# Kernel optimization log

Hardware: AMD Instinct MI355X
Metric: run time of the kernel (lower is better)

## Reference

```python
import jax, jax.numpy as jnp
import numpy as np

DIM = 768

def setup_inputs() -> dict:
    key = jax.random.key(0)
    k1, k2, k3, k4 = jax.random.split(key, 4)
    B, N, C = 32, 577, DIM
    x = jax.random.normal(k1, (B, N, C), dtype=jnp.float32)
    # torch Linear weights: (out_features, in_features)
    w_qkv = jax.random.normal(k2, (3 * C, C), dtype=jnp.float32) * (C ** -0.5)
    w_proj = jax.random.normal(k3, (C, C), dtype=jnp.float32) * (C ** -0.5)
    b_proj = jax.random.normal(k4, (C,), dtype=jnp.float32) * 0.02
    return {"x": x, "w_qkv": w_qkv, "w_proj": w_proj, "b_proj": b_proj}

def reference(x, w_qkv, w_proj, b_proj):
    B, N, C = x.shape
    attn_size = int((N - 1) ** 0.5)
    scale = C ** -0.5
    qkv = (x @ w_qkv.T).reshape(B, N, 3, C)          # [B,N,3,C]
    qkv = jnp.transpose(qkv, (2, 0, 1, 3))           # [3,B,N,C]
    q, k, v = qkv[0], qkv[1], qkv[2]
    attn = jax.nn.softmax(jnp.einsum('bnc,bmc->bnm', q, k) * scale, axis=-1)  # [B,N,N]
    y = jnp.einsum('bnm,bmc->bnc', attn, v)          # [B,N,C]
    # faithful to original: transpose(1,2) then reshape back (data permutation)
    y = jnp.transpose(y, (0, 2, 1)).reshape(B, N, C)
    out = y @ w_proj.T + b_proj
    token_attn = attn[:, 0, 1:].reshape(B, 1, attn_size, attn_size)
    return (out, token_attn)
```

## Files before the change

kernel.cpp:

```cpp
#include <hip/hip_runtime.h>


typedef __attribute__((ext_vector_type(4))) float f32x4;
typedef __attribute__((ext_vector_type(8))) short short8;
typedef __attribute__((ext_vector_type(8))) unsigned short ushort8v;
typedef __attribute__((ext_vector_type(4))) unsigned short ushort4v;

#define TILE 128
#define BK 64

#define NB 32
#define SEQ 577
#define SEQP 640
#define DIM 768
#define MTOT (NB * SEQ)
#define VTLD (NB * SEQP)
#define KC 0.05205949529797614f

__device__ __forceinline__ unsigned short f2bf(float f) {
  union { float f; unsigned u; } x; x.f = f;
  unsigned r = x.u + 0x7fffu + ((x.u >> 16) & 1u);
  return (unsigned short)(r >> 16);
}

__device__ __forceinline__ float bf2f(unsigned short v) {
  union { unsigned u; float f; } x; x.u = ((unsigned)v) << 16; return x.f;
}

__device__ __forceinline__ void gload16(const unsigned short* g, unsigned short* l) {
  __builtin_amdgcn_global_load_lds(
      (const __attribute__((address_space(1))) unsigned int*)g,
      (__attribute__((address_space(3))) unsigned int*)l, 16, 0, 0);
}

__device__ __forceinline__ int swiz(int lin, int nblk) {
  int xcd = lin & 7, pos = lin >> 3;
  int per = nblk >> 3, rem = nblk & 7;
  return xcd * per + (xcd < rem ? xcd : rem) + pos;
}

__device__ __forceinline__ void gemm_core(
    unsigned short* smem,
    const unsigned short* __restrict__ A, int ldA, int rowmaxA, int blkM,
    const unsigned short* __restrict__ B, int ldB, int rowmaxB, int blkN,
    int K, f32x4 acc[4][4])
{
  unsigned short* sA = smem;
  unsigned short* sB = smem + TILE * BK;
  const int t = threadIdx.x;
  const int lane = t & 63;
  const int wave = t >> 6;
  const int wr = (wave >> 1) * 64;
  const int wc = (wave & 1) * 64;
  const int lrow = lane & 15;
  const int quad = lane >> 4;

  for (int k0 = 0; k0 < K; k0 += BK) {
#pragma unroll
    for (int it = 0; it < 4; ++it) {
      int tt = t + it * 256;
      int rr = tt >> 3;
      int gc = (tt & 7) ^ (rr & 7);
      int ra = blkM + rr; if (ra > rowmaxA) ra = rowmaxA;
      int rb = blkN + rr; if (rb > rowmaxB) rb = rowmaxB;
      gload16(A + (size_t)ra * ldA + k0 + gc * 8, sA + tt * 8);
      gload16(B + (size_t)rb * ldB + k0 + gc * 8, sB + tt * 8);
    }
    __syncthreads();
#pragma unroll
    for (int kk = 0; kk < 2; ++kk) {
      short8 af[4], bfr[4];
#pragma unroll
      for (int i = 0; i < 4; ++i) {
        int m = wr + i * 16 + lrow;
        af[i] = *(const short8*)(sA + m * BK + (((kk * 4 + quad) ^ (m & 7)) * 8));
      }
#pragma unroll
      for (int j = 0; j < 4; ++j) {
        int n = wc + j * 16 + lrow;
        bfr[j] = *(const short8*)(sB + n * BK + (((kk * 4 + quad) ^ (n & 7)) * 8));
      }
#pragma unroll
      for (int i = 0; i < 4; ++i)
#pragma unroll
        for (int j = 0; j < 4; ++j)
          acc[i][j] = __builtin_amdgcn_mfma_f32_16x16x32_bf16(af[i], bfr[j], acc[i][j], 0, 0, 0);
    }
    __syncthreads();
  }
}

#define N4X  3545088
#define N4W1 442368
#define N4W2 147456
__global__ __launch_bounds__(256) void k_cvt3(
    const float* __restrict__ x, const float* __restrict__ w1, const float* __restrict__ w2,
    unsigned short* __restrict__ xo, unsigned short* __restrict__ w1o,
    unsigned short* __restrict__ w2o) {
  int i = blockIdx.x * 256 + threadIdx.x;
  const float4* src; ushort4* dst; int off;
  if (i < N4X)                 { src = (const float4*)x;  dst = (ushort4*)xo;  off = i; }
  else if (i < N4X + N4W1)     { src = (const float4*)w1; dst = (ushort4*)w1o; off = i - N4X; }
  else                         { src = (const float4*)w2; dst = (ushort4*)w2o; off = i - N4X - N4W1; }
  float4 v = src[off];
  ushort4 o;
  o.x = f2bf(v.x); o.y = f2bf(v.y); o.z = f2bf(v.z); o.w = f2bf(v.w);
  dst[off] = o;
}

__global__ __launch_bounds__(256, 2) void k_qkv(
    const unsigned short* __restrict__ xb, const unsigned short* __restrict__ wb,
    unsigned short* __restrict__ qb, unsigned short* __restrict__ kb,
    unsigned short* __restrict__ vt) {
  __shared__ unsigned short smem[2 * TILE * BK];
  f32x4 acc[4][4];
#pragma unroll
  for (int i = 0; i < 4; ++i)
#pragma unroll
    for (int j = 0; j < 4; ++j) acc[i][j] = (f32x4){0.f, 0.f, 0.f, 0.f};

  int lin = swiz(blockIdx.y * 18 + blockIdx.x, 18 * 160);
  const int tN = lin % 18;
  const int tMall = lin / 18;
  const int b = tMall / 5;
  const int mt = tMall % 5;
  const int sel = tN / 6, cbase = (tN % 6) * TILE;
  const unsigned short* Xb = xb + (size_t)b * SEQ * DIM;

  const int t = threadIdx.x, lane = t & 63, wave = t >> 6;
  const int wr = (wave >> 1) * 64, wc = (wave & 1) * 64;
  const int l15 = lane & 15, quad = lane >> 4;

  if (sel < 2) {
    gemm_core(smem, Xb, DIM, SEQ - 1, mt * TILE, wb, DIM, 3 * DIM - 1, tN * TILE, DIM, acc);
#pragma unroll
    for (int i = 0; i < 4; ++i)
#pragma unroll
      for (int j = 0; j < 4; ++j)
#pragma unroll
        for (int r = 0; r < 4; ++r) {
          int m = wr + i * 16 + quad * 4 + r, n = wc + j * 16 + l15;
          smem[m * TILE + (n ^ ((m & 7) << 3))] = f2bf(acc[i][j][r]);
        }
    __syncthreads();
    unsigned short* dst = sel == 0 ? qb : kb;
#pragma unroll
    for (int s = 0; s < 8; ++s) {
      int idx = t + s * 256, rr = idx >> 4, seg = idx & 15;
      int nn = mt * TILE + rr;
      if (nn < SEQ) {
        ushort8v v = *(const ushort8v*)(smem + rr * TILE + ((seg * 8) ^ ((rr & 7) << 3)));
        *(ushort8v*)(dst + ((size_t)(b * SEQ + nn)) * DIM + cbase + seg * 8) = v;
      }
    }
  } else {
    gemm_core(smem, wb, DIM, 3 * DIM - 1, 2 * DIM + cbase, Xb, DIM, SEQ - 1, mt * TILE, DIM, acc);
#pragma unroll
    for (int i = 0; i < 4; ++i)
#pragma unroll
      for (int j = 0; j < 4; ++j)
#pragma unroll
        for (int r = 0; r < 4; ++r) {
          int m = wr + i * 16 + quad * 4 + r, n = wc + j * 16 + l15;
          smem[m * TILE + (n ^ ((m & 7) << 3))] = f2bf(acc[i][j][r]);
        }
    __syncthreads();
#pragma unroll
    for (int s = 0; s < 8; ++s) {
      int idx = t + s * 256, rr = idx >> 4, seg = idx & 15;
      int c = cbase + rr;
      int n0 = mt * TILE + seg * 8;
      if (n0 < SEQ) {
        ushort8v v = *(const ushort8v*)(smem + rr * TILE + ((seg * 8) ^ ((rr & 7) << 3)));
        unsigned short* dp = vt + (size_t)c * VTLD + (size_t)b * SEQP + n0;
        if (n0 + 8 <= SEQ) *(ushort8v*)dp = v;
        else {
#pragma unroll
          for (int e = 0; e < 8; ++e) if (n0 + e < SEQ) dp[e] = v[e];
        }
      }
    }
  }
}

__global__ __launch_bounds__(256, 2) void k_logits(
    const unsigned short* __restrict__ qb, const unsigned short* __restrict__ kb,
    unsigned short* __restrict__ Pt, float* __restrict__ part) {
  __shared__ unsigned short smem[2 * TILE * BK];
  __shared__ float rpart[128][2];
  f32x4 acc[4][4];
#pragma unroll
  for (int i = 0; i < 4; ++i)
#pragma unroll
    for (int j = 0; j < 4; ++j) acc[i][j] = (f32x4){0.f, 0.f, 0.f, 0.f};
  int lin = swiz(blockIdx.y * 25 + blockIdx.x, 25 * NB);
  const int b = lin / 25;
  const int tM = (lin % 25) / 5, tN = lin % 5;
  const unsigned short* A = qb + (size_t)b * SEQ * DIM;
  const unsigned short* B = kb + (size_t)b * SEQ * DIM;
  gemm_core(smem, A, DIM, SEQ - 1, tM * TILE, B, DIM, SEQ - 1, tN * TILE, DIM, acc);

  const int t = threadIdx.x, lane = t & 63, wave = t >> 6;
  const int wr = (wave >> 1) * 64, wc = (wave & 1) * 64;
  const int l15 = lane & 15, quad = lane >> 4;

#pragma unroll
  for (int i = 0; i < 4; ++i)
#pragma unroll
    for (int j = 0; j < 4; ++j) {
      int ng = tN * TILE + wc + j * 16 + l15;
#pragma unroll
      for (int r = 0; r < 4; ++r) {
        float e = exp2f(acc[i][j][r] * KC);
        acc[i][j][r] = (ng < SEQ) ? e : 0.f;
      }
    }
#pragma unroll
  for (int i = 0; i < 4; ++i)
#pragma unroll
    for (int r = 0; r < 4; ++r) {
      float p = acc[i][0][r] + acc[i][1][r] + acc[i][2][r] + acc[i][3][r];
      p += __shfl_xor(p, 1); p += __shfl_xor(p, 2);
      p += __shfl_xor(p, 4); p += __shfl_xor(p, 8);
      if (l15 == 0) rpart[wr + i * 16 + quad * 4 + r][wave & 1] = p;
    }
  __syncthreads();
  if (t < 128) {
    int row = tM * TILE + t;
    part[((size_t)b * 5 + tN) * SEQP + row] = rpart[t][0] + rpart[t][1];
  }
#pragma unroll
  for (int i = 0; i < 4; ++i)
#pragma unroll
    for (int j = 0; j < 4; ++j)
#pragma unroll
      for (int r = 0; r < 4; ++r) {
        int m = wr + i * 16 + quad * 4 + r, n = wc + j * 16 + l15;
        smem[m * TILE + (n ^ ((m & 7) << 3))] = f2bf(acc[i][j][r]);
      }
  __syncthreads();
  unsigned short* Pb = Pt + (size_t)b * SEQP * SEQP;
#pragma unroll
  for (int s = 0; s < 8; ++s) {
    int idx = t + s * 256, rr = idx >> 4, seg = idx & 15;
    int m = tM * TILE + rr;
    ushort8v v = *(const ushort8v*)(smem + rr * TILE + ((seg * 8) ^ ((rr & 7) << 3)));
    *(ushort8v*)(Pb + (size_t)m * SEQP + tN * TILE + seg * 8) = v;
  }
}

__global__ __launch_bounds__(256, 2) void k_pv(
    const unsigned short* __restrict__ Pt, const unsigned short* __restrict__ vt,
    const float* __restrict__ part, unsigned short* __restrict__ yf,
    float* __restrict__ tok) {
  __shared__ unsigned short smem[2 * TILE * BK];
  __shared__ float linv[128];
  f32x4 acc[4][4];
#pragma unroll
  for (int i = 0; i < 4; ++i)
#pragma unroll
    for (int j = 0; j < 4; ++j) acc[i][j] = (f32x4){0.f, 0.f, 0.f, 0.f};
  int lin = swiz(blockIdx.y * 30 + blockIdx.x, 30 * NB);
  const int b = lin / 30;
  const int tC = (lin % 30) / 5, tT = lin % 5;
  gemm_core(smem, vt + (size_t)b * SEQP, VTLD, DIM - 1, tC * TILE,
            Pt + (size_t)b * SEQP * SEQP, SEQP, SEQP - 1, tT * TILE, SEQP, acc);

  const int t = threadIdx.x, lane = t & 63, wave = t >> 6;
  const int wr = (wave >> 1) * 64, wc = (wave & 1) * 64;
  const int l15 = lane & 15, quad = lane >> 4;

  if (t < 128) {
    int row = tT * TILE + t;
    const float* pp = part + (size_t)b * 5 * SEQP + row;
    float s = pp[0] + pp[SEQP] + pp[2 * SEQP] + pp[3 * SEQP] + pp[4 * SEQP];
    linv[t] = 1.0f / s;
  }
  __syncthreads();

#pragma unroll
  for (int j = 0; j < 4; ++j) {
    float ln = linv[wc + j * 16 + l15];
#pragma unroll
    for (int i = 0; i < 4; ++i)
#pragma unroll
      for (int r = 0; r < 4; ++r) {
        int m = wr + i * 16 + quad * 4 + r, n = wc + j * 16 + l15;
        smem[m * TILE + (n ^ ((m & 7) << 3))] = f2bf(acc[i][j][r] * ln);
      }
  }
  __syncthreads();

  const int rowc = t >> 1, h = t & 1;
  const int c = tC * TILE + rowc;
  const int sw = (rowc & 7) << 3;
  unsigned short* yrow = yf + ((size_t)b * DIM + c) * SEQ;
  int n0 = tT * TILE + h * 64;
  int nend = n0 + 64; if (nend > SEQ) nend = SEQ;
  int n = n0;
  while (n < nend && ((c + n) & 3)) { yrow[n] = smem[rowc * TILE + ((n - tT * TILE) ^ sw)]; ++n; }
  for (; n + 4 <= nend; n += 4) {
    ushort4v v;
#pragma unroll
    for (int e = 0; e < 4; ++e) v[e] = smem[rowc * TILE + ((n + e - tT * TILE) ^ sw)];
    *(ushort4v*)(yrow + n) = v;
  }
  for (; n < nend; ++n) yrow[n] = smem[rowc * TILE + ((n - tT * TILE) ^ sw)];

  if (tC == 0 && t < 128) {
    const float* pp = part + (size_t)b * 5 * SEQP;
    float inv0 = 1.0f / (pp[0] + pp[SEQP] + pp[2 * SEQP] + pp[3 * SEQP] + pp[4 * SEQP]);
    int nt = tT * TILE + t;
    if (nt >= 1 && nt < SEQ)
      tok[(size_t)b * (SEQ - 1) + nt - 1] =
          bf2f(Pt[(size_t)b * SEQP * SEQP + nt]) * inv0;
  }
}

__global__ __launch_bounds__(256, 2) void k_proj(
    const unsigned short* __restrict__ yf, const unsigned short* __restrict__ wpb,
    const float* __restrict__ bproj, float* __restrict__ out) {
  __shared__ unsigned short smem[2 * TILE * BK];
  f32x4 acc[4][4];
#pragma unroll
  for (int i = 0; i < 4; ++i)
#pragma unroll
    for (int j = 0; j < 4; ++j) acc[i][j] = (f32x4){0.f, 0.f, 0.f, 0.f};
  int lin = swiz(blockIdx.y * 6 + blockIdx.x, 6 * 145);
  const int tM = lin / 6, tN = lin % 6;
  gemm_core(smem, yf, DIM, MTOT - 1, tM * TILE, wpb, DIM, DIM - 1, tN * TILE, DIM, acc);

  const int t = threadIdx.x, lane = t & 63, wave = t >> 6;
  const int wc = (wave & 1) * 64;
  const int l15 = lane & 15, quad = lane >> 4;
  float* smem32 = (float*)smem;
  const int wquad = wave >> 1;

#pragma unroll
  for (int p = 0; p < 2; ++p) {
    if (wquad == p) {
#pragma unroll
      for (int j = 0; j < 4; ++j) {
        int n = wc + j * 16 + l15;
        float bias = bproj[tN * TILE + n];
#pragma unroll
        for (int i = 0; i < 4; ++i)
#pragma unroll
          for (int r = 0; r < 4; ++r)
            smem32[(i * 16 + quad * 4 + r) * TILE + n] = acc[i][j][r] + bias;
      }
    }
    __syncthreads();
#pragma unroll
    for (int s = 0; s < 8; ++s) {
      int idx = t + s * 256;
      int rloc = idx >> 5, col4 = idx & 31;
      int m = tM * TILE + p * 64 + rloc;
      if (m < MTOT)
        ((float4*)(out + (size_t)m * DIM + tN * TILE))[col4] =
            ((const float4*)(smem32 + rloc * TILE))[col4];
    }
    __syncthreads();
  }
}

extern "C" void kernel_launch(void* const* d_in, const int* in_sizes, int n_in,
                              void* d_out, int out_size, void* d_ws, size_t ws_size,
                              hipStream_t stream) {
  const float* x     = (const float*)d_in[0];
  const float* wqkv  = (const float*)d_in[1];
  const float* wproj = (const float*)d_in[2];
  const float* bproj = (const float*)d_in[3];
  float* out = (float*)d_out;
  float* tok = out + (size_t)NB * SEQ * DIM;

  char* ws = (char*)d_ws;
  unsigned short* xb    = (unsigned short*)(ws + 0);
  unsigned short* wqkvb = (unsigned short*)(ws + 28360704);
  unsigned short* wprojb= (unsigned short*)(ws + 31899648);
  unsigned short* qb    = (unsigned short*)(ws + 33079296);
  unsigned short* kb    = (unsigned short*)(ws + 61440000);
  unsigned short* vt    = (unsigned short*)(ws + 89800704);
  unsigned short* Pt    = (unsigned short*)(ws + 121257984);
  float*          part  = (float*)         (ws + 147472384);
  unsigned short* yf    = (unsigned short*)(ws + 147881984);

  k_cvt3<<<16152, 256, 0, stream>>>(x, wqkv, wproj, xb, wqkvb, wprojb);
  k_qkv<<<dim3(18, 160), 256, 0, stream>>>(xb, wqkvb, qb, kb, vt);
  k_logits<<<dim3(25, NB), 256, 0, stream>>>(qb, kb, Pt, part);
  k_pv<<<dim3(30, NB), 256, 0, stream>>>(Pt, vt, part, yf, tok);
  k_proj<<<dim3(6, 145), 256, 0, stream>>>(yf, wprojb, bproj, out);
}
```

Measured before the change: 298.4 us.

## Split QKV GEMM into flat Q/K GEMM and separate V-transpose kernel

```diff
diff --git a/kernel.cpp b/kernel.cpp
--- a/kernel.cpp
+++ b/kernel.cpp
@@ -108,9 +108,50 @@
   dst[off] = o;
 }
 
-__global__ __launch_bounds__(256, 2) void k_qkv(
+__global__ __launch_bounds__(256, 2) void k_qkv_qk(
     const unsigned short* __restrict__ xb, const unsigned short* __restrict__ wb,
-    unsigned short* __restrict__ qb, unsigned short* __restrict__ kb,
+    unsigned short* __restrict__ qb, unsigned short* __restrict__ kb) {
+  __shared__ unsigned short smem[2 * TILE * BK];
+  f32x4 acc[4][4];
+#pragma unroll
+  for (int i = 0; i < 4; ++i)
+#pragma unroll
+    for (int j = 0; j < 4; ++j) acc[i][j] = (f32x4){0.f, 0.f, 0.f, 0.f};
+
+  int lin = swiz(blockIdx.y * 12 + blockIdx.x, 12 * 145);
+  const int tN = lin % 12;
+  const int tM = lin / 12;
+  const int sel = tN / 6, cbase = (tN % 6) * TILE;
+  gemm_core(smem, xb, DIM, MTOT - 1, tM * TILE, wb, DIM, 3 * DIM - 1, tN * TILE, DIM, acc);
+
+  const int t = threadIdx.x, lane = t & 63, wave = t >> 6;
+  const int wr = (wave >> 1) * 64, wc = (wave & 1) * 64;
+  const int l15 = lane & 15, quad = lane >> 4;
+
+#pragma unroll
+  for (int i = 0; i < 4; ++i)
+#pragma unroll
+    for (int j = 0; j < 4; ++j)
+#pragma unroll
+      for (int r = 0; r < 4; ++r) {
+        int m = wr + i * 16 + quad * 4 + r, n = wc + j * 16 + l15;
+        smem[m * TILE + (n ^ ((m & 7) << 3))] = f2bf(acc[i][j][r]);
+      }
+  __syncthreads();
+  unsigned short* dst = sel == 0 ? qb : kb;
+#pragma unroll
+  for (int s = 0; s < 8; ++s) {
+    int idx = t + s * 256, rr = idx >> 4, seg = idx & 15;
+    int m = tM * TILE + rr;
+    if (m < MTOT) {
+      ushort8v v = *(const ushort8v*)(smem + rr * TILE + ((seg * 8) ^ ((rr & 7) << 3)));
+      *(ushort8v*)(dst + (size_t)m * DIM + cbase + seg * 8) = v;
+    }
+  }
+}
+
+__global__ __launch_bounds__(256, 2) void k_qkv_v(
+    const unsigned short* __restrict__ xb, const unsigned short* __restrict__ wb,
     unsigned short* __restrict__ vt) {
   __shared__ unsigned short smem[2 * TILE * BK];
   f32x4 acc[4][4];
@@ -119,65 +160,39 @@
 #pragma unroll
     for (int j = 0; j < 4; ++j) acc[i][j] = (f32x4){0.f, 0.f, 0.f, 0.f};
 
-  int lin = swiz(blockIdx.y * 18 + blockIdx.x, 18 * 160);
-  const int tN = lin % 18;
-  const int tMall = lin / 18;
-  const int b = tMall / 5;
-  const int mt = tMall % 5;
-  const int sel = tN / 6, cbase = (tN % 6) * TILE;
+  int lin = swiz(blockIdx.y * 6 + blockIdx.x, 6 * 160);
+  const int ct = lin % 6;
+  const int rest = lin / 6;
+  const int b = rest / 5, mt = rest % 5;
   const unsigned short* Xb = xb + (size_t)b * SEQ * DIM;
+  gemm_core(smem, wb, DIM, 3 * DIM - 1, 2 * DIM + ct * TILE, Xb, DIM, SEQ - 1, mt * TILE, DIM, acc);
 
   const int t = threadIdx.x, lane = t & 63, wave = t >> 6;
   const int wr = (wave >> 1) * 64, wc = (wave & 1) * 64;
   const int l15 = lane & 15, quad = lane >> 4;
 
-  if (sel < 2) {
-    gemm_core(smem, Xb, DIM, SEQ - 1, mt * TILE, wb, DIM, 3 * DIM - 1, tN * TILE, DIM, acc);
-#pragma unroll
-    for (int i = 0; i < 4; ++i)
-#pragma unroll
-      for (int j = 0; j < 4; ++j)
-#pragma unroll
-        for (int r = 0; r < 4; ++r) {
-          int m = wr + i * 16 + quad * 4 + r, n = wc + j * 16 + l15;
-          smem[m * TILE + (n ^ ((m & 7) << 3))] = f2bf(acc[i][j][r]);
-        }
-    __syncthreads();
-    unsigned short* dst = sel == 0 ? qb : kb;
-#pragma unroll
-    for (int s = 0; s < 8; ++s) {
-      int idx = t + s * 256, rr = idx >> 4, seg = idx & 15;
-      int nn = mt * TILE + rr;
-      if (nn < SEQ) {
-        ushort8v v = *(const ushort8v*)(smem + rr * TILE + ((seg * 8) ^ ((rr & 7) << 3)));
-        *(ushort8v*)(dst + ((size_t)(b * SEQ + nn)) * DIM + cbase + seg * 8) = v;
-      }
-    }
-  } else {
-    gemm_core(smem, wb, DIM, 3 * DIM - 1, 2 * DIM + cbase, Xb, DIM, SEQ - 1, mt * TILE, DIM, acc);
-#pragma unroll
-    for (int i = 0; i < 4; ++i)
-#pragma unroll
-      for (int j = 0; j < 4; ++j)
-#pragma unroll
-        for (int r = 0; r < 4; ++r) {
-          int m = wr + i * 16 + quad * 4 + r, n = wc + j * 16 + l15;
-          smem[m * TILE + (n ^ ((m & 7) << 3))] = f2bf(acc[i][j][r]);
-        }
-    __syncthreads();
-#pragma unroll
-    for (int s = 0; s < 8; ++s) {
-      int idx = t + s * 256, rr = idx >> 4, seg = idx & 15;
-      int c = cbase + rr;
-      int n0 = mt * TILE + seg * 8;
-      if (n0 < SEQ) {
-        ushort8v v = *(const ushort8v*)(smem + rr * TILE + ((seg * 8) ^ ((rr & 7) << 3)));
-        unsigned short* dp = vt + (size_t)c * VTLD + (size_t)b * SEQP + n0;
-        if (n0 + 8 <= SEQ) *(ushort8v*)dp = v;
-        else {
-#pragma unroll
-          for (int e = 0; e < 8; ++e) if (n0 + e < SEQ) dp[e] = v[e];
-        }
+#pragma unroll
+  for (int i = 0; i < 4; ++i)
+#pragma unroll
+    for (int j = 0; j < 4; ++j)
+#pragma unroll
+      for (int r = 0; r < 4; ++r) {
+        int m = wr + i * 16 + quad * 4 + r, n = wc + j * 16 + l15;
+        smem[m * TILE + (n ^ ((m & 7) << 3))] = f2bf(acc[i][j][r]);
+      }
+  __syncthreads();
+#pragma unroll
+  for (int s = 0; s < 8; ++s) {
+    int idx = t + s * 256, rr = idx >> 4, seg = idx & 15;
+    int c = ct * TILE + rr;
+    int n0 = mt * TILE + seg * 8;
+    if (n0 < SEQ) {
+      ushort8v v = *(const ushort8v*)(smem + rr * TILE + ((seg * 8) ^ ((rr & 7) << 3)));
+      unsigned short* dp = vt + (size_t)c * VTLD + (size_t)b * SEQP + n0;
+      if (n0 + 8 <= SEQ) *(ushort8v*)dp = v;
+      else {
+#pragma unroll
+        for (int e = 0; e < 8; ++e) if (n0 + e < SEQ) dp[e] = v[e];
       }
     }
   }
@@ -227,7 +242,8 @@
   __syncthreads();
   if (t < 128) {
     int row = tM * TILE + t;
-    part[((size_t)b * 5 + tN) * SEQP + row] = rpart[t][0] + rpart[t][1];
+    if (row < SEQ)
+      part[((size_t)b * 5 + tN) * SEQP + row] = rpart[t][0] + rpart[t][1];
   }
 #pragma unroll
   for (int i = 0; i < 4; ++i)
@@ -244,8 +260,10 @@
   for (int s = 0; s < 8; ++s) {
     int idx = t + s * 256, rr = idx >> 4, seg = idx & 15;
     int m = tM * TILE + rr;
-    ushort8v v = *(const ushort8v*)(smem + rr * TILE + ((seg * 8) ^ ((rr & 7) << 3)));
-    *(ushort8v*)(Pb + (size_t)m * SEQP + tN * TILE + seg * 8) = v;
+    if (m < SEQ) {
+      ushort8v v = *(const ushort8v*)(smem + rr * TILE + ((seg * 8) ^ ((rr & 7) << 3)));
+      *(ushort8v*)(Pb + (size_t)m * SEQP + tN * TILE + seg * 8) = v;
+    }
   }
 }
 
@@ -272,9 +290,11 @@
 
   if (t < 128) {
     int row = tT * TILE + t;
-    const float* pp = part + (size_t)b * 5 * SEQP + row;
-    float s = pp[0] + pp[SEQP] + pp[2 * SEQP] + pp[3 * SEQP] + pp[4 * SEQP];
-    linv[t] = 1.0f / s;
+    if (row < SEQ) {
+      const float* pp = part + (size_t)b * 5 * SEQP + row;
+      float s = pp[0] + pp[SEQP] + pp[2 * SEQP] + pp[3 * SEQP] + pp[4 * SEQP];
+      linv[t] = 1.0f / s;
+    } else linv[t] = 0.0f;
   }
   __syncthreads();
 
@@ -386,8 +406,9 @@
   unsigned short* yf    = (unsigned short*)(ws + 147881984);
 
   k_cvt3<<<16152, 256, 0, stream>>>(x, wqkv, wproj, xb, wqkvb, wprojb);
-  k_qkv<<<dim3(18, 160), 256, 0, stream>>>(xb, wqkvb, qb, kb, vt);
+  k_qkv_qk<<<dim3(12, 145), 256, 0, stream>>>(xb, wqkvb, qb, kb);
   k_logits<<<dim3(25, NB), 256, 0, stream>>>(qb, kb, Pt, part);
+  k_qkv_v<<<dim3(6, 160), 256, 0, stream>>>(xb, wqkvb, vt);
   k_pv<<<dim3(30, NB), 256, 0, stream>>>(Pt, vt, part, yf, tok);
   k_proj<<<dim3(6, 145), 256, 0, stream>>>(yf, wprojb, bproj, out);
 }
```

Measured after the change: 298.5 us. Within noise of the previous version (+0.0%).
